# Kernel optimization log

Measured on AMD Instinct MI355X. Metric: run time of the kernel, lower is better.

The kernel has to match this reference:

```python
import jax, jax.numpy as jnp
import numpy as np

N = 200000   # total nodes across batch
E = 800000   # total edges (avg degree 4)
G = 64       # number of graphs in batch
NGT = 30     # num gate types
EMB = 64     # gate_type_embed_dim
H = 128      # h_feats
INTER = 128  # inter_dim
EPS = 1e-12  # F.normalize eps


def _xavier(key, shape):
    fan_in, fan_out = shape
    std = np.sqrt(2.0 / (fan_in + fan_out))
    return jax.random.normal(key, shape, dtype=jnp.float32) * std


def setup_inputs() -> dict:
    key = jax.random.key(0)
    ks = jax.random.split(key, 12)
    gate_type = jax.random.randint(ks[0], (N,), 0, NGT)
    src = jax.random.randint(ks[1], (E,), 0, N)
    dst = jax.random.randint(ks[2], (E,), 0, N)
    w = jax.random.uniform(ks[3], (E, 3), dtype=jnp.float32)
    node2graph = (jnp.arange(N) * G) // N  # sorted segment ids, even split
    emb = jax.random.normal(ks[4], (NGT, EMB), dtype=jnp.float32)
    return {
        "gate_type": gate_type, "src": src, "dst": dst, "w": w,
        "node2graph": node2graph, "emb": emb,
        "W1_0": _xavier(ks[5], (EMB + 3, INTER)), "b1_0": jnp.zeros((INTER,), jnp.float32),
        "W2_0": _xavier(ks[6], (EMB + INTER, H)),
        "W1_1": _xavier(ks[7], (H + 3, INTER)), "b1_1": jnp.zeros((INTER,), jnp.float32),
        "W2_1": _xavier(ks[8], (H + INTER, H)),
        "W1_2": _xavier(ks[9], (H + 3, INTER)), "b1_2": jnp.zeros((INTER,), jnp.float32),
        "W2_2": _xavier(ks[10], (H + INTER, H)),
    }


def _qconv(h, src, dst, w, W1, b1, W2):
    # message: cat(h[src], w) per edge; linear1+ReLU per message; sum per dst node
    m = jnp.concatenate([h[src], w], axis=1)          # [E, in+3]
    t = jax.nn.relu(m @ W1 + b1)                      # [E, inter]
    h_N = jax.ops.segment_sum(t, dst, num_segments=h.shape[0])  # [N, inter]
    h_lin = jax.nn.relu(jnp.concatenate([h, h_N], axis=1) @ W2)  # [N, out]
    norm = jnp.linalg.norm(h_lin, axis=-1, keepdims=True)
    return h_lin / jnp.maximum(norm, EPS)             # F.normalize(p=2, dim=-1)


def reference(gate_type, src, dst, w, node2graph, emb,
              W1_0, b1_0, W2_0, W1_1, b1_1, W2_1, W1_2, b1_2, W2_2):
    h = emb[gate_type]                                # [N, EMB]
    layers = [(W1_0, b1_0, W2_0), (W1_1, b1_1, W2_1), (W1_2, b1_2, W2_2)]
    readouts = []
    for W1, b1, W2 in layers:
        h = _qconv(h, src, dst, w, W1, b1, W2)
        readouts.append(jax.ops.segment_sum(h, node2graph, num_segments=G))  # [G, H]
    return h, jnp.concatenate(readouts, axis=1)       # [N,H], [G, 3H]
```

## Files before the change

### kernel.cpp

```cpp
#include <hip/hip_runtime.h>
#include <hip/hip_bf16.h>
#include <hip/hip_fp16.h>

typedef _Float16 half8 __attribute__((ext_vector_type(8)));
typedef _Float16 half4 __attribute__((ext_vector_type(4)));
typedef _Float16 h2    __attribute__((ext_vector_type(2)));
typedef float floatx4 __attribute__((ext_vector_type(4)));

__device__ __forceinline__ _Float16 f2h(float f) { return (_Float16)f; }


__global__ void fill_dummy_kernel(int4* __restrict__ eData, int cap, int N, int NGT)
{
    int i = blockIdx.x * 256 + threadIdx.x;
    if (i < cap) { int4 v = {N | (NGT << 24), N, 0, 0}; eData[i] = v; }
}

__global__ void hist_kernel(const int* __restrict__ dst, int* __restrict__ cnt, int E)
{
    int e = blockIdx.x * 256 + threadIdx.x;
    if (e < E) atomicAdd(&cnt[dst[e]], 1);
}

__global__ void scan1p_kernel(const int* __restrict__ cnt, int* __restrict__ offP,
                              int n, int* __restrict__ blockSums)
{
    __shared__ int sm[256];
    const int t = threadIdx.x;
    const int base = blockIdx.x * 1024 + t * 4;
    int v[4]; int s = 0;
#pragma unroll
    for (int i = 0; i < 4; ++i) {
        v[i] = (base + i < n) ? ((cnt[base + i] + 3) & ~3) : 0;
        s += v[i];
    }
    sm[t] = s; __syncthreads();
#pragma unroll
    for (int off = 1; off < 256; off <<= 1) {
        int y = (t >= off) ? sm[t - off] : 0;
        __syncthreads();
        if (t >= off) sm[t] += y;
        __syncthreads();
    }
    int excl = sm[t] - s;
    if (t == 255) blockSums[blockIdx.x] = sm[255];
    int run = excl;
#pragma unroll
    for (int i = 0; i < 4; ++i) {
        if (base + i < n) offP[base + i] = run;
        run += v[i];
    }
}

__global__ void scan2_kernel(int* __restrict__ blockSums, int nb)
{
    __shared__ int sm[256];
    const int t = threadIdx.x;
    int s = (t < nb) ? blockSums[t] : 0;
    sm[t] = s; __syncthreads();
#pragma unroll
    for (int off = 1; off < 256; off <<= 1) {
        int y = (t >= off) ? sm[t - off] : 0;
        __syncthreads();
        if (t >= off) sm[t] += y;
        __syncthreads();
    }
    if (t < nb) blockSums[t] = sm[t] - s;
}

__global__ void scan3_kernel(int* __restrict__ offP, int n, const int* __restrict__ blockSums)
{
    const int base = blockIdx.x * 1024 + threadIdx.x * 4;
    const int add = blockSums[blockIdx.x];
#pragma unroll
    for (int i = 0; i < 4; ++i)
        if (base + i < n) offP[base + i] += add;
}

__global__ void scatter_kernel(const int* __restrict__ src, const int* __restrict__ dst,
                               const float* __restrict__ w, const int* __restrict__ gt,
                               const int* __restrict__ offP, int* __restrict__ cur,
                               int4* __restrict__ eData, int E)
{
    int e = blockIdx.x * 256 + threadIdx.x;
    if (e >= E) return;
    int d = dst[e];
    int p = offP[d] + atomicAdd(&cur[d], 1);
    int s = src[e];
    h2 w01 = { f2h(w[(size_t)e * 3 + 0]), f2h(w[(size_t)e * 3 + 1]) };
    h2 w2o = { f2h(w[(size_t)e * 3 + 2]), (_Float16)1.0f };
    int4 v = { s | (gt[s] << 24), d,
               __builtin_bit_cast(int, w01), __builtin_bit_cast(int, w2o) };
    eData[p] = v;
}

__global__ void ginfo_kernel(const int4* __restrict__ eData,
                             const int* __restrict__ cnt, const int* __restrict__ offP,
                             unsigned* __restrict__ gInfo,
                             int nGroups, int N, int gpw)
{
    int g = blockIdx.x * 256 + threadIdx.x;
    if (g >= nGroups) return;
    const int* ei = (const int*)eData;
    int d = ei[16 * g + 1];
    if (d >= N) { gInfo[g] = 0xFFFFFFFFu; return; }
    int cntP = (cnt[d] + 3) & ~3;
    int gA = offP[d] >> 2;
    int gB = gA + (cntP >> 2) - 1;
    bool cross = (gA / gpw) != (gB / gpw);
    gInfo[g] = (unsigned)d | (cross ? 0x80000000u : 0u);
}

__global__ void wprep_kernel(const float* __restrict__ W, _Float16* __restrict__ out,
                             int K, int KP)
{
    int idx = blockIdx.x * 256 + threadIdx.x;
    if (idx >= 128 * KP) return;
    int f = idx / KP, k = idx % KP;
    float v = (k < K) ? W[(size_t)k * 128 + f] : 0.0f;
    out[idx] = f2h(v);
}

__global__ void wwprep_kernel(const float* __restrict__ W1, int rowOff,
                              _Float16* __restrict__ out)
{
    int idx = blockIdx.x * 256 + threadIdx.x;
    if (idx < 3 * 128) out[idx] = f2h(W1[(size_t)(rowOff + idx / 128) * 128 + (idx & 127)]);
}

__global__ void embW1_kernel(const float* __restrict__ emb, const float* __restrict__ W1,
                             const float* __restrict__ b1, _Float16* __restrict__ out, int NGT)
{
    int idx = blockIdx.x * 256 + threadIdx.x;
    if (idx >= (NGT + 1) * 128) return;
    int g = idx >> 7, f = idx & 127;
    float s = 0.0f;
    if (g < NGT) {
        s = b1[f];
        for (int k = 0; k < 64; ++k) s += emb[g * 64 + k] * W1[(size_t)k * 128 + f];
    }
    out[idx] = f2h(s);
}

__global__ void embW2_kernel(const float* __restrict__ emb, const float* __restrict__ W2,
                             float* __restrict__ out, int NGT)
{
    int idx = blockIdx.x * 256 + threadIdx.x;
    if (idx >= NGT * 128) return;
    int g = idx >> 7, f = idx & 127;
    float s = 0.0f;
    for (int k = 0; k < 64; ++k) s += emb[g * 64 + k] * W2[(size_t)k * 128 + f];
    out[idx] = s;
}

__global__ void __launch_bounds__(512, 2)
hw1_kernel(const _Float16* __restrict__ hA,
           const _Float16* __restrict__ WT,
           const float* __restrict__ b1,
           _Float16* __restrict__ out,
           int N, int tilesPerWave, int nTiles)
{
    __shared__ __align__(16) _Float16 lds[128 * 128];
    const int tid = threadIdx.x;
    for (int s = tid; s < 128 * 16; s += 512) {
        const int row = s / 16, seg = s % 16;
        half8 v = *(const half8*)(WT + (size_t)row * 128 + seg * 8);
        *(half8*)(&lds[row * 128 + ((seg ^ (row & 7)) * 8)]) = v;
    }
    __syncthreads();

    const int lane = tid & 63;
    const int wv   = tid >> 6;
    const int lRow = lane & 15;
    const int lGrp = lane >> 4;

    float b1v[8];
#pragma unroll
    for (int jt = 0; jt < 8; ++jt) b1v[jt] = b1[jt * 16 + lRow];

    const int wave = blockIdx.x * 8 + wv;
    const int t0 = wave * tilesPerWave;
    const int t1 = min(t0 + tilesPerWave, nTiles);

    for (int tile = t0; tile < t1; ++tile) {
        const int i0 = tile * 16;
        const int iA = min(i0 + lRow, N - 1);
        half8 a[4];
#pragma unroll
        for (int kc = 0; kc < 4; ++kc)
            a[kc] = *(const half8*)(hA + (size_t)iA * 128 + kc * 32 + lGrp * 8);

        floatx4 acc[8] = {};
#pragma unroll
        for (int jt = 0; jt < 8; ++jt) {
            const int row = jt * 16 + lRow;
            const int sw = row & 7;
#pragma unroll
            for (int kc = 0; kc < 4; ++kc) {
                half8 b = *(const half8*)(&lds[row * 128 + (((kc * 4 + lGrp) ^ sw) * 8)]);
                acc[jt] = __builtin_amdgcn_mfma_f32_16x16x32_f16(a[kc], b, acc[jt], 0, 0, 0);
            }
        }
#pragma unroll
        for (int r = 0; r < 4; ++r) {
            const int i = i0 + lGrp * 4 + r;
            if (i < N) {
#pragma unroll
                for (int jt = 0; jt < 8; ++jt)
                    out[(size_t)i * 128 + jt * 16 + lRow] = f2h(acc[jt][r] + b1v[jt]);
            }
        }
    }
}

template<bool L0, bool H16>
__global__ void __launch_bounds__(256, 4)
edgeW_kernel(const _Float16* __restrict__ T,
             const _Float16* __restrict__ Wwh,
             const int4* __restrict__ eData,
             const unsigned* __restrict__ gInfo,
             void* __restrict__ hNv, int groupsPerWave, int nGroups)
{
    const int tid  = threadIdx.x;
    const int lane = tid & 63;
    const int wv   = tid >> 6;
    const int sub  = lane >> 5;
    const int col4 = (lane & 31) * 4;

    const h2 z = {(_Float16)0.0f, (_Float16)0.0f};
    const h2 w0a = *(const h2*)(Wwh + 0 * 128 + col4);
    const h2 w0b = *(const h2*)(Wwh + 0 * 128 + col4 + 2);
    const h2 w1a = *(const h2*)(Wwh + 1 * 128 + col4);
    const h2 w1b = *(const h2*)(Wwh + 1 * 128 + col4 + 2);
    const h2 w2a = *(const h2*)(Wwh + 2 * 128 + col4);
    const h2 w2b = *(const h2*)(Wwh + 2 * 128 + col4 + 2);

    const int wave = blockIdx.x * 4 + wv;
    const int g0 = wave * groupsPerWave;
    const int g1 = min(g0 + groupsPerWave, nGroups);
    if (g0 >= g1) return;

    int runD = -1; bool runCross = false;
    h2 a0 = z, a1 = z;

    auto flush = [&]() {
        if (runD < 0) return;
        h2 s0 = a0, s1 = a1;
        int o0 = __shfl_xor(__builtin_bit_cast(int, s0), 32);
        int o1 = __shfl_xor(__builtin_bit_cast(int, s1), 32);
        s0 = s0 + __builtin_bit_cast(h2, o0);
        s1 = s1 + __builtin_bit_cast(h2, o1);
        if (lane < 32) {
            if (H16) {
                if (runCross) {
                    __half2* a0p = (__half2*)((__half*)hNv + (size_t)runD * 128 + col4);
                    unsafeAtomicAdd(a0p, __builtin_bit_cast(__half2, s0));
                    unsafeAtomicAdd(a0p + 1, __builtin_bit_cast(__half2, s1));
                } else {
                    int2 pk = { __builtin_bit_cast(int, s0), __builtin_bit_cast(int, s1) };
                    *(int2*)((__half*)hNv + (size_t)runD * 128 + col4) = pk;
                }
            } else {
                float f0 = (float)s0[0], f1 = (float)s0[1];
                float f2 = (float)s1[0], f3 = (float)s1[1];
                float* a0p = (float*)hNv + (size_t)runD * 128 + col4;
                if (runCross) {
                    unsafeAtomicAdd(a0p + 0, f0); unsafeAtomicAdd(a0p + 1, f1);
                    unsafeAtomicAdd(a0p + 2, f2); unsafeAtomicAdd(a0p + 3, f3);
                } else {
                    floatx4 p = {f0, f1, f2, f3};
                    *(floatx4*)a0p = p;
                }
            }
        }
    };

    for (int g = g0; g < g1; ++g) {
        const unsigned gi = gInfo[g];
        if (gi == 0xFFFFFFFFu) break;
        const int dG = (int)(gi & 0xFFFFFFu);
        const int4 ea = eData[g * 4 + sub];
        const int4 eb = eData[g * 4 + 2 + sub];
        const int ra = L0 ? (ea.x >> 24) : (ea.x & 0xFFFFFF);
        const int rb = L0 ? (eb.x >> 24) : (eb.x & 0xFFFFFF);
        const h2 wa01 = __builtin_bit_cast(h2, ea.z);
        const h2 wa2o = __builtin_bit_cast(h2, ea.w);
        const h2 wb01 = __builtin_bit_cast(h2, eb.z);
        const h2 wb2o = __builtin_bit_cast(h2, eb.w);
        const half4 Tav = *(const half4*)(T + (size_t)ra * 128 + col4);
        const half4 Tbv = *(const half4*)(T + (size_t)rb * 128 + col4);
        const h2 Ta0 = {Tav[0], Tav[1]}, Ta1 = {Tav[2], Tav[3]};
        const h2 Tb0 = {Tbv[0], Tbv[1]}, Tb1 = {Tbv[2], Tbv[3]};

        h2 ma0 = Ta0 + wa01[0] * w0a + wa01[1] * w1a + wa2o[0] * w2a;
        h2 ma1 = Ta1 + wa01[0] * w0b + wa01[1] * w1b + wa2o[0] * w2b;
        h2 mb0 = Tb0 + wb01[0] * w0a + wb01[1] * w1a + wb2o[0] * w2a;
        h2 mb1 = Tb1 + wb01[0] * w0b + wb01[1] * w1b + wb2o[0] * w2b;
        h2 r0 = __builtin_elementwise_max(ma0, z) + __builtin_elementwise_max(mb0, z);
        h2 r1 = __builtin_elementwise_max(ma1, z) + __builtin_elementwise_max(mb1, z);

        if (dG == runD) {
            a0 = a0 + r0; a1 = a1 + r1;
        } else {
            flush();
            runD = dG; runCross = (gi >> 31) != 0;
            a0 = r0; a1 = r1;
        }
    }
    flush();
}

template<bool H16, bool L0, bool LAST>
__global__ void __launch_bounds__(512, 2)
node_kernel(const _Float16* __restrict__ hA,
            const void* __restrict__ hNv,
            const _Float16* __restrict__ W2T,
            const float* __restrict__ embW2,
            const int* __restrict__ gt,
            const int* __restrict__ n2g,
            _Float16* __restrict__ hOut,
            float* __restrict__ fOut,
            float* __restrict__ readout,
            int N, int tilesPerWave, int nTiles, int layerOff)
{
    constexpr int K2  = L0 ? 128 : 256;
    constexpr int KCA = L0 ? 0 : 4;
    constexpr int KC  = K2 / 32;
    constexpr int SPR = K2 / 8;
    __shared__ __align__(16) _Float16 lds[128 * K2];

    const int tid = threadIdx.x;
    for (int s = tid; s < 128 * SPR; s += 512) {
        const int row = s / SPR, seg = s % SPR;
        half8 v = *(const half8*)(W2T + (size_t)row * K2 + seg * 8);
        *(half8*)(&lds[row * K2 + ((seg ^ (row & 7)) * 8)]) = v;
    }
    __syncthreads();

    const int lane = tid & 63;
    const int wv   = tid >> 6;
    const int lRow = lane & 15;
    const int lGrp = lane >> 4;
    const int wave = blockIdx.x * 8 + wv;
    const int t0 = wave * tilesPerWave;
    const int t1 = min(t0 + tilesPerWave, nTiles);
    if (t0 >= t1) return;

    int gCur = -1; float racc[8];
#pragma unroll
    for (int jt = 0; jt < 8; ++jt) racc[jt] = 0.0f;

    auto loadA = [&](int i0, half8 (&afrag)[KC]) {
        const int iA = min(i0 + lRow, N - 1);
#pragma unroll
        for (int kc = 0; kc < KCA; ++kc)
            afrag[kc] = *(const half8*)(hA + (size_t)iA * 128 + kc * 32 + lGrp * 8);
        if (H16) {
            const _Float16* hN = (const _Float16*)hNv;
#pragma unroll
            for (int kc = KCA; kc < KC; ++kc)
                afrag[kc] = *(const half8*)(hN + (size_t)iA * 128 + (kc - KCA) * 32 + lGrp * 8);
        } else {
            const float* hN = (const float*)hNv;
#pragma unroll
            for (int kc = KCA; kc < KC; ++kc) {
                const float* p = hN + (size_t)iA * 128 + (kc - KCA) * 32 + lGrp * 8;
                floatx4 f0 = *(const floatx4*)(p);
                floatx4 f1 = *(const floatx4*)(p + 4);
                half8 a;
#pragma unroll
                for (int i = 0; i < 4; ++i) { a[i] = f2h(f0[i]); a[i + 4] = f2h(f1[i]); }
                afrag[kc] = a;
            }
        }
    };

    auto epilogue = [&](int i0, floatx4 (&acc)[8]) {
        if (L0) {
#pragma unroll
            for (int r = 0; r < 4; ++r) {
                const int i = min(i0 + lGrp * 4 + r, N - 1);
                const int g_t = gt[i];
#pragma unroll
                for (int jt = 0; jt < 8; ++jt)
                    acc[jt][r] += embW2[(size_t)g_t * 128 + jt * 16 + lRow];
            }
        }
        float scl[4];
#pragma unroll
        for (int r = 0; r < 4; ++r) {
            float s = 0.f;
#pragma unroll
            for (int jt = 0; jt < 8; ++jt) {
                float v = fmaxf(acc[jt][r], 0.0f);
                s += v * v;
            }
#pragma unroll
            for (int m = 1; m <= 8; m <<= 1) s += __shfl_xor(s, m);
            scl[r] = 1.0f / fmaxf(sqrtf(s), 1e-12f);
        }
#pragma unroll
        for (int r = 0; r < 4; ++r) {
            const int i = i0 + lGrp * 4 + r;
            if (i < N) {
#pragma unroll
                for (int jt = 0; jt < 8; ++jt) {
                    float v = fmaxf(acc[jt][r], 0.0f) * scl[r];
                    if (LAST) fOut[(size_t)i * 128 + jt * 16 + lRow] = v;
                    else      hOut[(size_t)i * 128 + jt * 16 + lRow] = f2h(v);
                }
            }
        }
        const int gFirst = n2g[min(i0, N - 1)];
        const int gLast  = n2g[min(i0 + 15, N - 1)];
        if (gFirst == gLast && i0 + 15 < N) {
            if (gFirst != gCur) {
                if (gCur >= 0 && lane < 16) {
#pragma unroll
                    for (int jt = 0; jt < 8; ++jt)
                        unsafeAtomicAdd(&readout[(size_t)gCur * 384 + layerOff + jt * 16 + lane], racc[jt]);
                }
                gCur = gFirst;
#pragma unroll
                for (int jt = 0; jt < 8; ++jt) racc[jt] = 0.0f;
            }
#pragma unroll
            for (int jt = 0; jt < 8; ++jt) {
                float t = 0.f;
#pragma unroll
                for (int r = 0; r < 4; ++r) t += fmaxf(acc[jt][r], 0.0f) * scl[r];
                t += __shfl_xor(t, 16);
                t += __shfl_xor(t, 32);
                racc[jt] += t;
            }
        } else {
            if (gCur >= 0 && lane < 16) {
#pragma unroll
                for (int jt = 0; jt < 8; ++jt)
                    unsafeAtomicAdd(&readout[(size_t)gCur * 384 + layerOff + jt * 16 + lane], racc[jt]);
            }
            gCur = -1;
#pragma unroll
            for (int jt = 0; jt < 8; ++jt) racc[jt] = 0.0f;
#pragma unroll
            for (int r = 0; r < 4; ++r) {
                const int i = i0 + lGrp * 4 + r;
                if (i < N) {
                    const int g = n2g[i];
#pragma unroll
                    for (int jt = 0; jt < 8; ++jt) {
                        float v = fmaxf(acc[jt][r], 0.0f) * scl[r];
                        unsafeAtomicAdd(&readout[(size_t)g * 384 + layerOff + jt * 16 + lRow], v);
                    }
                }
            }
        }
    };

    for (int tile = t0; tile < t1; tile += 2) {
        const bool has2 = (tile + 1 < t1);
        const int i0a = tile * 16;
        const int i0b = has2 ? (tile + 1) * 16 : i0a;

        half8 afA[KC], afB[KC];
        loadA(i0a, afA);
        loadA(i0b, afB);

        floatx4 accA[8] = {}, accB[8] = {};
#pragma unroll
        for (int jt = 0; jt < 8; ++jt) {
            const int rb = (jt * 16 + lRow) * K2;
            const int sw = (jt * 16 + lRow) & 7;
#pragma unroll
            for (int kc = 0; kc < KC; ++kc) {
                half8 b = *(const half8*)(&lds[rb + (((kc * 4 + lGrp) ^ sw) * 8)]);
                accA[jt] = __builtin_amdgcn_mfma_f32_16x16x32_f16(afA[kc], b, accA[jt], 0, 0, 0);
                accB[jt] = __builtin_amdgcn_mfma_f32_16x16x32_f16(afB[kc], b, accB[jt], 0, 0, 0);
            }
        }
        epilogue(i0a, accA);
        if (has2) epilogue(i0b, accB);
    }
    if (gCur >= 0 && lane < 16) {
#pragma unroll
        for (int jt = 0; jt < 8; ++jt)
            unsafeAtomicAdd(&readout[(size_t)gCur * 384 + layerOff + jt * 16 + lane], racc[jt]);
    }
}

extern "C" void kernel_launch(void* const* d_in, const int* in_sizes, int n_in,
                              void* d_out, int out_size, void* d_ws, size_t ws_size,
                              hipStream_t stream)
{
    const int*   gate_type = (const int*)d_in[0];
    const int*   src  = (const int*)d_in[1];
    const int*   dst  = (const int*)d_in[2];
    const float* wE   = (const float*)d_in[3];
    const int*   n2g  = (const int*)d_in[4];
    const float* emb  = (const float*)d_in[5];
    const float* W1_0 = (const float*)d_in[6];
    const float* b1_0 = (const float*)d_in[7];
    const float* W2_0 = (const float*)d_in[8];
    const float* W1_1 = (const float*)d_in[9];
    const float* b1_1 = (const float*)d_in[10];
    const float* W2_1 = (const float*)d_in[11];
    const float* W1_2 = (const float*)d_in[12];
    const float* b1_2 = (const float*)d_in[13];
    const float* W2_2 = (const float*)d_in[14];

    const int N = in_sizes[0];
    const int E = in_sizes[1];
    const int NGT = in_sizes[5] / 64;
    const int cap = (E + 3 * N + 15) & ~15;

    char* ws = (char*)d_ws;
    size_t off = 0;
    auto alloc = [&](size_t bytes) { void* p = ws + off; off = (off + bytes + 255) & ~255ULL; return p; };
    _Float16* hBuf  = (_Float16*)alloc((size_t)N * 128 * 2);
    int4*     eData = (int4*)alloc(((size_t)cap + 16) * 16);
    unsigned* gInfo = (unsigned*)alloc(((size_t)cap / 4 + 4) * 4);
    int*      cnt   = (int*)alloc((size_t)N * 4);
    int*      offP  = (int*)alloc((size_t)N * 4);
    int*      cur   = (int*)alloc((size_t)N * 4);
    int*      bSums = (int*)alloc(256 * 4);
    _Float16* W1T1  = (_Float16*)alloc((size_t)128 * 128 * 2);
    _Float16* W1T2  = (_Float16*)alloc((size_t)128 * 128 * 2);
    _Float16* W2T0  = (_Float16*)alloc((size_t)128 * 128 * 2);
    _Float16* W2T1  = (_Float16*)alloc((size_t)128 * 256 * 2);
    _Float16* W2T2  = (_Float16*)alloc((size_t)128 * 256 * 2);
    _Float16* Wwh0  = (_Float16*)alloc((size_t)3 * 128 * 2);
    _Float16* Wwh1  = (_Float16*)alloc((size_t)3 * 128 * 2);
    _Float16* Wwh2  = (_Float16*)alloc((size_t)3 * 128 * 2);
    _Float16* eW1b  = (_Float16*)alloc((size_t)(NGT + 1) * 128 * 2);
    float*    eW2   = (float*)alloc((size_t)NGT * 128 * 4);
    _Float16* hW1b  = (_Float16*)alloc(((size_t)N + 1) * 128 * 2);
    size_t hn16_off = off;
    const bool h16 = (ws_size >= hn16_off + (size_t)N * 128 * 2 + 256);
    _Float16* hN16 = (_Float16*)alloc((size_t)N * 128 * 2);

    float* readout = (float*)d_out + (size_t)N * 128;
    void*  hN      = h16 ? (void*)hN16 : (void*)d_out;

    const int nGroups = cap / 4;
    const int nTiles  = (N + 15) / 16;
    const int EB = 2048;
    const int gpw = (nGroups + EB * 4 - 1) / (EB * 4);
    const int NB = 256;
    const int tpwN = (nTiles + NB * 8 - 1) / (NB * 8);
    const int HB = 256;
    const int tpwH = (nTiles + HB * 8 - 1) / (HB * 8);
    const int nb = (N + 1023) / 1024;

    hipMemsetAsync(cnt, 0, (size_t)N * 4, stream);
    hipMemsetAsync(cur, 0, (size_t)N * 4, stream);
    hipMemsetAsync(hW1b + (size_t)N * 128, 0, 256, stream);
    fill_dummy_kernel<<<(cap + 16 + 255) / 256, 256, 0, stream>>>(eData, cap + 16, N, NGT);
    hist_kernel<<<(E + 255) / 256, 256, 0, stream>>>(dst, cnt, E);
    scan1p_kernel<<<nb, 256, 0, stream>>>(cnt, offP, N, bSums);
    scan2_kernel<<<1, 256, 0, stream>>>(bSums, nb);
    scan3_kernel<<<nb, 256, 0, stream>>>(offP, N, bSums);
    scatter_kernel<<<(E + 255) / 256, 256, 0, stream>>>(src, dst, wE, gate_type,
                                                        offP, cur, eData, E);
    ginfo_kernel<<<(nGroups + 255) / 256, 256, 0, stream>>>(eData, cnt, offP, gInfo,
                                                            nGroups, N, gpw);

    embW1_kernel<<<((NGT + 1) * 128 + 255) / 256, 256, 0, stream>>>(emb, W1_0, b1_0, eW1b, NGT);
    embW2_kernel<<<(NGT * 128 + 255) / 256, 256, 0, stream>>>(emb, W2_0, eW2, NGT);
    wprep_kernel<<<(128 * 128 + 255) / 256, 256, 0, stream>>>(W1_1, W1T1, 128, 128);
    wprep_kernel<<<(128 * 128 + 255) / 256, 256, 0, stream>>>(W1_2, W1T2, 128, 128);
    wprep_kernel<<<(128 * 128 + 255) / 256, 256, 0, stream>>>(W2_0 + (size_t)64 * 128, W2T0, 128, 128);
    wprep_kernel<<<(128 * 256 + 255) / 256, 256, 0, stream>>>(W2_1, W2T1, 256, 256);
    wprep_kernel<<<(128 * 256 + 255) / 256, 256, 0, stream>>>(W2_2, W2T2, 256, 256);
    wwprep_kernel<<<2, 256, 0, stream>>>(W1_0, 64, Wwh0);
    wwprep_kernel<<<2, 256, 0, stream>>>(W1_1, 128, Wwh1);
    wwprep_kernel<<<2, 256, 0, stream>>>(W1_2, 128, Wwh2);

    if (h16) {
        hipMemsetAsync(readout, 0, (size_t)(out_size - N * 128) * 4, stream);
        hipMemsetAsync(hN16, 0, (size_t)N * 128 * 2, stream);
        edgeW_kernel<true, true><<<EB, 256, 0, stream>>>(eW1b, Wwh0, eData, gInfo, hN, gpw, nGroups);
        node_kernel<true, true, false><<<NB, 512, 0, stream>>>(nullptr, hN, W2T0, eW2, gate_type, n2g,
                                                               hBuf, nullptr, readout, N, tpwN, nTiles, 0);
        hw1_kernel<<<HB, 512, 0, stream>>>(hBuf, W1T1, b1_1, hW1b, N, tpwH, nTiles);
        hipMemsetAsync(hN16, 0, (size_t)N * 128 * 2, stream);
        edgeW_kernel<false, true><<<EB, 256, 0, stream>>>(hW1b, Wwh1, eData, gInfo, hN, gpw, nGroups);
        node_kernel<true, false, false><<<NB, 512, 0, stream>>>(hBuf, hN, W2T1, nullptr, nullptr, n2g,
                                                                hBuf, nullptr, readout, N, tpwN, nTiles, 128);
        hw1_kernel<<<HB, 512, 0, stream>>>(hBuf, W1T2, b1_2, hW1b, N, tpwH, nTiles);
        hipMemsetAsync(hN16, 0, (size_t)N * 128 * 2, stream);
        edgeW_kernel<false, true><<<EB, 256, 0, stream>>>(hW1b, Wwh2, eData, gInfo, hN, gpw, nGroups);
        node_kernel<true, false, true><<<NB, 512, 0, stream>>>(hBuf, hN, W2T2, nullptr, nullptr, n2g,
                                                               nullptr, (float*)d_out, readout, N, tpwN, nTiles, 256);
    } else {
        hipMemsetAsync(d_out, 0, (size_t)out_size * 4, stream);
        edgeW_kernel<true, false><<<EB, 256, 0, stream>>>(eW1b, Wwh0, eData, gInfo, hN, gpw, nGroups);
        node_kernel<false, true, false><<<NB, 512, 0, stream>>>(nullptr, hN, W2T0, eW2, gate_type, n2g,
                                                                hBuf, nullptr, readout, N, tpwN, nTiles, 0);
        hw1_kernel<<<HB, 512, 0, stream>>>(hBuf, W1T1, b1_1, hW1b, N, tpwH, nTiles);
        hipMemsetAsync(d_out, 0, (size_t)N * 128 * 4, stream);
        edgeW_kernel<false, false><<<EB, 256, 0, stream>>>(hW1b, Wwh1, eData, gInfo, hN, gpw, nGroups);
        node_kernel<false, false, false><<<NB, 512, 0, stream>>>(hBuf, hN, W2T1, nullptr, nullptr, n2g,
                                                                 hBuf, nullptr, readout, N, tpwN, nTiles, 128);
        hw1_kernel<<<HB, 512, 0, stream>>>(hBuf, W1T2, b1_2, hW1b, N, tpwH, nTiles);
        hipMemsetAsync(d_out, 0, (size_t)N * 128 * 4, stream);
        edgeW_kernel<false, false><<<EB, 256, 0, stream>>>(hW1b, Wwh2, eData, gInfo, hN, gpw, nGroups);
        node_kernel<false, false, true><<<NB, 512, 0, stream>>>(hBuf, hN, W2T2, nullptr, nullptr, n2g,
                                                                nullptr, (float*)d_out, readout, N, tpwN, nTiles, 256);
    }
}
```

Measured before the change: 507.7 us.

## Give each destination node single-wave ownership and zero only empty rows

New measurement: 515.0 us. Within noise of the previous version (+1.4%).

```diff
diff --git a/kernel.cpp b/kernel.cpp
--- a/kernel.cpp
+++ b/kernel.cpp
@@ -94,21 +94,31 @@
     eData[p] = v;
 }
 
-__global__ void ginfo_kernel(const int4* __restrict__ eData,
-                             const int* __restrict__ cnt, const int* __restrict__ offP,
-                             unsigned* __restrict__ gInfo,
-                             int nGroups, int N, int gpw)
+__global__ void ginfo_kernel(const int4* __restrict__ eData, unsigned* __restrict__ gInfo,
+                             int nGroups, int N)
 {
     int g = blockIdx.x * 256 + threadIdx.x;
     if (g >= nGroups) return;
-    const int* ei = (const int*)eData;
-    int d = ei[16 * g + 1];
-    if (d >= N) { gInfo[g] = 0xFFFFFFFFu; return; }
-    int cntP = (cnt[d] + 3) & ~3;
-    int gA = offP[d] >> 2;
-    int gB = gA + (cntP >> 2) - 1;
-    bool cross = (gA / gpw) != (gB / gpw);
-    gInfo[g] = (unsigned)d | (cross ? 0x80000000u : 0u);
+    int d = ((const int*)eData)[16 * g + 1];
+    gInfo[g] = (d >= N) ? 0xFFFFFFFFu : (unsigned)d;
+}
+
+__global__ void zlist_kernel(const int* __restrict__ cnt, int* __restrict__ zCnt,
+                             int* __restrict__ zList, int N)
+{
+    int d = blockIdx.x * 256 + threadIdx.x;
+    if (d < N && cnt[d] == 0) zList[atomicAdd(zCnt, 1)] = d;
+}
+
+__global__ void zero_rows_kernel(const int* __restrict__ zList, const int* __restrict__ zCnt,
+                                 _Float16* __restrict__ hN)
+{
+    const int n = *zCnt * 16;
+    for (int i = blockIdx.x * 256 + threadIdx.x; i < n; i += gridDim.x * 256) {
+        const int row = zList[i >> 4], c = (i & 15) * 8;
+        int4 zz = {0, 0, 0, 0};
+        *(int4*)(hN + (size_t)row * 128 + c) = zz;
+    }
 }
 
 __global__ void wprep_kernel(const float* __restrict__ W, _Float16* __restrict__ out,
@@ -237,10 +247,19 @@
 
     const int wave = blockIdx.x * 4 + wv;
     const int g0 = wave * groupsPerWave;
+    if (g0 >= nGroups) return;
     const int g1 = min(g0 + groupsPerWave, nGroups);
-    if (g0 >= g1) return;
-
-    int runD = -1; bool runCross = false;
+
+    int g = g0;
+    {
+        unsigned gi0 = gInfo[g0];
+        if (gi0 == 0xFFFFFFFFu) return;
+        if (g0 > 0 && gInfo[g0 - 1] == gi0) {
+            do { ++g; } while (g < nGroups && gInfo[g] == gi0);
+        }
+    }
+
+    int runD = -1;
     h2 a0 = z, a1 = z;
 
     auto flush = [&]() {
@@ -252,33 +271,20 @@
         s1 = s1 + __builtin_bit_cast(h2, o1);
         if (lane < 32) {
             if (H16) {
-                if (runCross) {
-                    __half2* a0p = (__half2*)((__half*)hNv + (size_t)runD * 128 + col4);
-                    unsafeAtomicAdd(a0p, __builtin_bit_cast(__half2, s0));
-                    unsafeAtomicAdd(a0p + 1, __builtin_bit_cast(__half2, s1));
-                } else {
-                    int2 pk = { __builtin_bit_cast(int, s0), __builtin_bit_cast(int, s1) };
-                    *(int2*)((__half*)hNv + (size_t)runD * 128 + col4) = pk;
-                }
+                int2 pk = { __builtin_bit_cast(int, s0), __builtin_bit_cast(int, s1) };
+                *(int2*)((__half*)hNv + (size_t)runD * 128 + col4) = pk;
             } else {
-                float f0 = (float)s0[0], f1 = (float)s0[1];
-                float f2 = (float)s1[0], f3 = (float)s1[1];
-                float* a0p = (float*)hNv + (size_t)runD * 128 + col4;
-                if (runCross) {
-                    unsafeAtomicAdd(a0p + 0, f0); unsafeAtomicAdd(a0p + 1, f1);
-                    unsafeAtomicAdd(a0p + 2, f2); unsafeAtomicAdd(a0p + 3, f3);
-                } else {
-                    floatx4 p = {f0, f1, f2, f3};
-                    *(floatx4*)a0p = p;
-                }
+                floatx4 p = {(float)s0[0], (float)s0[1], (float)s1[0], (float)s1[1]};
+                *(floatx4*)((float*)hNv + (size_t)runD * 128 + col4) = p;
             }
         }
     };
 
-    for (int g = g0; g < g1; ++g) {
+    while (g < nGroups) {
         const unsigned gi = gInfo[g];
         if (gi == 0xFFFFFFFFu) break;
-        const int dG = (int)(gi & 0xFFFFFFu);
+        const int dG = (int)gi;
+        if (g >= g1 && dG != runD) break;
         const int4 ea = eData[g * 4 + sub];
         const int4 eb = eData[g * 4 + 2 + sub];
         const int ra = L0 ? (ea.x >> 24) : (ea.x & 0xFFFFFF);
@@ -303,9 +309,10 @@
             a0 = a0 + r0; a1 = a1 + r1;
         } else {
             flush();
-            runD = dG; runCross = (gi >> 31) != 0;
+            runD = dG;
             a0 = r0; a1 = r1;
         }
+        ++g;
     }
     flush();
 }
@@ -523,6 +530,8 @@
     int*      offP  = (int*)alloc((size_t)N * 4);
     int*      cur   = (int*)alloc((size_t)N * 4);
     int*      bSums = (int*)alloc(256 * 4);
+    int*      zCnt  = (int*)alloc(256);
+    int*      zList = (int*)alloc((size_t)N * 4);
     _Float16* W1T1  = (_Float16*)alloc((size_t)128 * 128 * 2);
     _Float16* W1T2  = (_Float16*)alloc((size_t)128 * 128 * 2);
     _Float16* W2T0  = (_Float16*)alloc((size_t)128 * 128 * 2);
@@ -553,6 +562,7 @@
 
     hipMemsetAsync(cnt, 0, (size_t)N * 4, stream);
     hipMemsetAsync(cur, 0, (size_t)N * 4, stream);
+    hipMemsetAsync(zCnt, 0, 4, stream);
     hipMemsetAsync(hW1b + (size_t)N * 128, 0, 256, stream);
     fill_dummy_kernel<<<(cap + 16 + 255) / 256, 256, 0, stream>>>(eData, cap + 16, N, NGT);
     hist_kernel<<<(E + 255) / 256, 256, 0, stream>>>(dst, cnt, E);
@@ -561,8 +571,8 @@
     scan3_kernel<<<nb, 256, 0, stream>>>(offP, N, bSums);
     scatter_kernel<<<(E + 255) / 256, 256, 0, stream>>>(src, dst, wE, gate_type,
                                                         offP, cur, eData, E);
-    ginfo_kernel<<<(nGroups + 255) / 256, 256, 0, stream>>>(eData, cnt, offP, gInfo,
-                                                            nGroups, N, gpw);
+    ginfo_kernel<<<(nGroups + 255) / 256, 256, 0, stream>>>(eData, gInfo, nGroups, N);
+    zlist_kernel<<<(N + 255) / 256, 256, 0, stream>>>(cnt, zCnt, zList, N);
 
     embW1_kernel<<<((NGT + 1) * 128 + 255) / 256, 256, 0, stream>>>(emb, W1_0, b1_0, eW1b, NGT);
     embW2_kernel<<<(NGT * 128 + 255) / 256, 256, 0, stream>>>(emb, W2_0, eW2, NGT);
@@ -577,17 +587,15 @@
 
     if (h16) {
         hipMemsetAsync(readout, 0, (size_t)(out_size - N * 128) * 4, stream);
-        hipMemsetAsync(hN16, 0, (size_t)N * 128 * 2, stream);
+        zero_rows_kernel<<<128, 256, 0, stream>>>(zList, zCnt, hN16);
         edgeW_kernel<true, true><<<EB, 256, 0, stream>>>(eW1b, Wwh0, eData, gInfo, hN, gpw, nGroups);
         node_kernel<true, true, false><<<NB, 512, 0, stream>>>(nullptr, hN, W2T0, eW2, gate_type, n2g,
                                                                hBuf, nullptr, readout, N, tpwN, nTiles, 0);
         hw1_kernel<<<HB, 512, 0, stream>>>(hBuf, W1T1, b1_1, hW1b, N, tpwH, nTiles);
-        hipMemsetAsync(hN16, 0, (size_t)N * 128 * 2, stream);
         edgeW_kernel<false, true><<<EB, 256, 0, stream>>>(hW1b, Wwh1, eData, gInfo, hN, gpw, nGroups);
         node_kernel<true, false, false><<<NB, 512, 0, stream>>>(hBuf, hN, W2T1, nullptr, nullptr, n2g,
                                                                 hBuf, nullptr, readout, N, tpwN, nTiles, 128);
         hw1_kernel<<<HB, 512, 0, stream>>>(hBuf, W1T2, b1_2, hW1b, N, tpwH, nTiles);
-        hipMemsetAsync(hN16, 0, (size_t)N * 128 * 2, stream);
         edgeW_kernel<false, true><<<EB, 256, 0, stream>>>(hW1b, Wwh2, eData, gInfo, hN, gpw, nGroups);
         node_kernel<true, false, true><<<NB, 512, 0, stream>>>(hBuf, hN, W2T2, nullptr, nullptr, n2g,
                                                                nullptr, (float*)d_out, readout, N, tpwN, nTiles, 256);
```
